# Kernel optimization log

Measured on AMD Instinct MI355X. Metric: run time of the kernel, lower is better.

## Reference

```python
import jax, jax.numpy as jnp
import numpy as np

BOUND = 5.0      # zuko MonotonicRQSTransform default bound
SLOPE = 1e-4     # minimum derivative slope
BINS = 5
HIDDEN = [128, 128, 128, 128]
N = 524288


def setup_inputs() -> dict:
    key = jax.random.key(0)
    ks = jax.random.split(key, 16)
    x = jax.random.normal(ks[0], (N, 1), dtype=jnp.float32)   # context
    z = jax.random.normal(ks[1], (N, 1), dtype=jnp.float32)   # base-normal sample
    dims = [1] + HIDDEN + [3 * BINS - 1]  # conditioner MLP: 1 -> 128x4 -> 14
    inp = {"x": x, "z": z}
    for i, (din, dout) in enumerate(zip(dims[:-1], dims[1:])):
        inp[f"W{i}"] = jax.random.normal(ks[2 + 2 * i], (din, dout), jnp.float32) / np.sqrt(din).astype(np.float32)
        inp[f"b{i}"] = jax.random.normal(ks[3 + 2 * i], (dout,), jnp.float32) * 0.01
    return inp


def _mlp(c, Ws, bs):
    h = c
    for W, b in zip(Ws[:-1], bs[:-1]):
        h = jax.nn.relu(h @ W + b)
    return h @ Ws[-1] + bs[-1]


def _rqs_inverse(z, w_raw, h_raw, d_raw):
    """Inverse of the monotonic rational-quadratic spline (Durkan et al. 2019).
    z: [N]; w_raw,h_raw: [N,K]; d_raw: [N,K-1]. Identity outside [-B, B]."""
    widths = 2.0 * BOUND * jax.nn.softmax(w_raw, axis=-1)
    heights = 2.0 * BOUND * jax.nn.softmax(h_raw, axis=-1)
    xk = -BOUND + jnp.pad(jnp.cumsum(widths, -1), ((0, 0), (1, 0)))   # [N,K+1] x-knots
    yk = -BOUND + jnp.pad(jnp.cumsum(heights, -1), ((0, 0), (1, 0)))  # [N,K+1] y-knots
    dk = jnp.pad(SLOPE + jax.nn.softplus(d_raw), ((0, 0), (1, 1)), constant_values=1.0)  # [N,K+1]

    zc = jnp.clip(z, -BOUND, BOUND)
    # bin search over K=5 inner knots via comparison-sum
    k = jnp.clip(jnp.sum(zc[:, None] >= yk[:, 1:-1], axis=-1), 0, BINS - 1)  # [N]
    take = lambda a: jnp.take_along_axis(a, k[:, None], axis=-1)[:, 0]
    x0, x1 = take(xk[:, :-1]), take(xk[:, 1:])
    y0, y1 = take(yk[:, :-1]), take(yk[:, 1:])
    d0, d1 = take(dk[:, :-1]), take(dk[:, 1:])

    dx, dy = x1 - x0, y1 - y0
    s = dy / dx
    t = zc - y0
    m = d0 + d1 - 2.0 * s
    a = dy * (s - d0) + t * m
    b = dy * d0 - t * m
    c = -s * t
    disc = jnp.maximum(b * b - 4.0 * a * c, 0.0)
    xi = 2.0 * c / (-b - jnp.sqrt(disc))  # stable quadratic root in [0,1]
    x_in = x0 + xi * dx
    return jnp.where(jnp.abs(z) >= BOUND, z, x_in)


def reference(x, z, W0, b0, W1, b1, W2, b2, W3, b3, W4, b4):
    # NICE with features=1: masks [T],[F],[T] -> transforms 0 & 2 are identity;
    # only transform 1 is active, conditioned on the context alone.
    Ws = [W0, W1, W2, W3, W4]
    bs = [b0, b1, b2, b3, b4]
    phi = _mlp(x, Ws, bs)  # [N, 3*BINS-1]
    w_raw = phi[:, :BINS]
    h_raw = phi[:, BINS:2 * BINS]
    d_raw = phi[:, 2 * BINS:]
    y = _rqs_inverse(z[:, 0], w_raw, h_raw, d_raw)  # sample = T^{-1}(z)
    return y[:, None]
```

## Files before the change

### kernel.cpp

```cpp
#include <hip/hip_runtime.h>

typedef _Float16 half8 __attribute__((ext_vector_type(8)));
typedef _Float16 half2v __attribute__((ext_vector_type(2)));
typedef __fp16   fp16x2 __attribute__((ext_vector_type(2)));
typedef float    f32x4 __attribute__((ext_vector_type(4)));


__global__ __launch_bounds__(256) void prep_kernel(
    const float* __restrict__ W1, const float* __restrict__ W2,
    const float* __restrict__ W3, const float* __restrict__ W4,
    const float* __restrict__ W0, const float* __restrict__ b0,
    _Float16* __restrict__ out)
{
    int t = blockIdx.x * blockDim.x + threadIdx.x;
    if (t >= 6912) return;
    int lane = t & 63;
    int frag = t >> 6;
    int col  = lane & 15;
    int kq   = (lane >> 4) << 2;

    if (frag < 96) {
        int l = frag >> 5, f = frag & 31;
        const float* W = (l == 0) ? W1 : (l == 1) ? W2 : W3;
        int mt = f >> 2, ks = f & 3;
        _Float16* dst = out + l * 16384 + f * 512 + lane * 8;
        int m = mt * 16 + col;
        int kbase = ks * 32 + kq;
#pragma unroll
        for (int j = 0; j < 8; ++j) {
            int k = kbase + 16 * (j >> 2) + (j & 3);
            dst[j] = (_Float16)W[k * 128 + m];
        }
    } else if (frag < 100) {
        int ks = frag - 96;
        _Float16* dst = out + 49152 + ks * 512 + lane * 8;
        int m = col;
        int kbase = ks * 32 + kq;
#pragma unroll
        for (int j = 0; j < 8; ++j) {
            int k = kbase + 16 * (j >> 2) + (j & 3);
            float v = (m < 14) ? W4[k * 14 + m] : 0.0f;
            dst[j] = (_Float16)v;
        }
    } else {
        int mt = frag - 100;
        _Float16* dst = out + 53248 + mt * 512 + lane * 8;
        int m = mt * 16 + col;
#pragma unroll
        for (int j = 0; j < 8; ++j) {
            int k = 16 * (j >> 2) + kq + (j & 3);
            float v = (k == 0) ? W0[m] : (k == 1) ? b0[m] : 0.0f;
            dst[j] = (_Float16)v;
        }
    }
}

static __device__ __forceinline__ half2v relu_cvt2(float a, float b) {
    fp16x2 h = __builtin_amdgcn_cvt_pkrtz(a, b);
    fp16x2 zz = {(__fp16)0.0f, (__fp16)0.0f};
    h = __builtin_elementwise_max(h, zz);
    return __builtin_bit_cast(half2v, h);
}

static __device__ __forceinline__ void hidden_layer(
    const half8 (&bin)[4][4], half8 (&bout)[4][4],
    const float* __restrict__ bias, const _Float16* __restrict__ Al,
    int lane, int quad)
{
#pragma unroll
    for (int mtp = 0; mtp < 4; ++mtp) {
        f32x4 acc[4][2];
        half8 a[2][4];
#pragma unroll
        for (int h = 0; h < 2; ++h) {
            int mt = 2 * mtp + h;
            f32x4 bv = *(const f32x4*)(bias + mt * 16 + quad * 4);
#pragma unroll
            for (int g = 0; g < 4; ++g) acc[g][h] = bv;
#pragma unroll
            for (int ks = 0; ks < 4; ++ks)
                a[h][ks] = *(const half8*)(Al + (mt * 4 + ks) * 512 + lane * 8);
        }
        __builtin_amdgcn_s_setprio(1);
#pragma unroll
        for (int h = 0; h < 2; ++h)
#pragma unroll
            for (int ks = 0; ks < 4; ++ks)
#pragma unroll
                for (int g = 0; g < 4; ++g)
                    acc[g][h] = __builtin_amdgcn_mfma_f32_16x16x32_f16(a[h][ks], bin[g][ks], acc[g][h], 0, 0, 0);
        __builtin_amdgcn_s_setprio(0);
#pragma unroll
        for (int g = 0; g < 4; ++g) {
            half2v p0 = relu_cvt2(acc[g][0][0], acc[g][0][1]);
            half2v p1 = relu_cvt2(acc[g][0][2], acc[g][0][3]);
            half2v p2 = relu_cvt2(acc[g][1][0], acc[g][1][1]);
            half2v p3 = relu_cvt2(acc[g][1][2], acc[g][1][3]);
            bout[g][mtp][0] = p0[0]; bout[g][mtp][1] = p0[1];
            bout[g][mtp][2] = p1[0]; bout[g][mtp][3] = p1[1];
            bout[g][mtp][4] = p2[0]; bout[g][mtp][5] = p2[1];
            bout[g][mtp][6] = p3[0]; bout[g][mtp][7] = p3[1];
        }
    }
}

__global__ __launch_bounds__(256, 2) void nflow_kernel(
    const float* __restrict__ x, const float* __restrict__ z,
    const float* __restrict__ b1, const float* __restrict__ b2,
    const float* __restrict__ b3, const float* __restrict__ b4v,
    const _Float16* __restrict__ Af, float* __restrict__ y, int N)
{
    __shared__ float phis[256][20];

    const int tid  = threadIdx.x;
    const int lane = tid & 63;
    const int wid  = tid >> 6;
    const int col  = lane & 15;
    const int quad = lane >> 4;
    const int sbase = blockIdx.x * 256 + wid * 64;

    half8 bufA[4][4], bufB[4][4];

    {
        half8 bx[4];
#pragma unroll
        for (int g = 0; g < 4; ++g) {
            int s = sbase + g * 16 + col;
            float xv = (s < N) ? x[s] : 0.0f;
            half8 t = {};
            if (quad == 0) { t[0] = (_Float16)xv; t[1] = (_Float16)1.0f; }
            bx[g] = t;
        }
#pragma unroll
        for (int mtp = 0; mtp < 4; ++mtp) {
            f32x4 acc[4][2];
            half8 a[2];
#pragma unroll
            for (int h = 0; h < 2; ++h)
                a[h] = *(const half8*)(Af + 53248 + (2 * mtp + h) * 512 + lane * 8);
            __builtin_amdgcn_s_setprio(1);
#pragma unroll
            for (int h = 0; h < 2; ++h)
#pragma unroll
                for (int g = 0; g < 4; ++g)
                    acc[g][h] = __builtin_amdgcn_mfma_f32_16x16x32_f16(a[h], bx[g], (f32x4){0.f,0.f,0.f,0.f}, 0, 0, 0);
            __builtin_amdgcn_s_setprio(0);
#pragma unroll
            for (int g = 0; g < 4; ++g) {
                half2v p0 = relu_cvt2(acc[g][0][0], acc[g][0][1]);
                half2v p1 = relu_cvt2(acc[g][0][2], acc[g][0][3]);
                half2v p2 = relu_cvt2(acc[g][1][0], acc[g][1][1]);
                half2v p3 = relu_cvt2(acc[g][1][2], acc[g][1][3]);
                bufA[g][mtp][0] = p0[0]; bufA[g][mtp][1] = p0[1];
                bufA[g][mtp][2] = p1[0]; bufA[g][mtp][3] = p1[1];
                bufA[g][mtp][4] = p2[0]; bufA[g][mtp][5] = p2[1];
                bufA[g][mtp][6] = p3[0]; bufA[g][mtp][7] = p3[1];
            }
        }
    }

    hidden_layer(bufA, bufB, b1, Af,         lane, quad);
    hidden_layer(bufB, bufA, b2, Af + 16384, lane, quad);
    hidden_layer(bufA, bufB, b3, Af + 32768, lane, quad);

    {
        f32x4 acc4[4];
        f32x4 binit;
#pragma unroll
        for (int r = 0; r < 4; ++r) {
            int comp = quad * 4 + r;
            binit[r] = (comp < 14) ? b4v[comp] : 0.0f;
        }
#pragma unroll
        for (int g = 0; g < 4; ++g) acc4[g] = binit;
        __builtin_amdgcn_s_setprio(1);
#pragma unroll
        for (int ks = 0; ks < 4; ++ks) {
            half8 a = *(const half8*)(Af + 49152 + ks * 512 + lane * 8);
#pragma unroll
            for (int g = 0; g < 4; ++g)
                acc4[g] = __builtin_amdgcn_mfma_f32_16x16x32_f16(a, bufB[g][ks], acc4[g], 0, 0, 0);
        }
        __builtin_amdgcn_s_setprio(0);
#pragma unroll
        for (int g = 0; g < 4; ++g)
            *(f32x4*)&phis[wid * 64 + g * 16 + col][quad * 4] = acc4[g];
    }

    __syncthreads();

    {
        int gs = blockIdx.x * 256 + tid;
        if (gs < N) {
            float ph[16];
            *(f32x4*)&ph[0]  = *(const f32x4*)&phis[tid][0];
            *(f32x4*)&ph[4]  = *(const f32x4*)&phis[tid][4];
            *(f32x4*)&ph[8]  = *(const f32x4*)&phis[tid][8];
            *(f32x4*)&ph[12] = *(const f32x4*)&phis[tid][12];

            float mw = ph[0], mh = ph[5];
#pragma unroll
            for (int i = 1; i < 5; ++i) { mw = fmaxf(mw, ph[i]); mh = fmaxf(mh, ph[5 + i]); }
            float ew[5], eh[5];
            float sw = 0.f, sh = 0.f;
#pragma unroll
            for (int i = 0; i < 5; ++i) {
                ew[i] = __expf(ph[i] - mw);      sw += ew[i];
                eh[i] = __expf(ph[5 + i] - mh);  sh += eh[i];
            }
            float iw = 10.0f / sw, ih = 10.0f / sh;
            float xk[6], yk[6], dk[6];
            xk[0] = -5.0f; yk[0] = -5.0f;
#pragma unroll
            for (int i = 0; i < 5; ++i) {
                xk[i + 1] = xk[i] + ew[i] * iw;
                yk[i + 1] = yk[i] + eh[i] * ih;
            }
            dk[0] = 1.0f; dk[5] = 1.0f;
#pragma unroll
            for (int i = 0; i < 4; ++i) {
                float v = ph[10 + i];
                dk[i + 1] = 0.0001f + fmaxf(v, 0.0f) + __logf(1.0f + __expf(-fabsf(v)));
            }
            float zv = z[gs];
            float zc = fminf(fmaxf(zv, -5.0f), 5.0f);
            int k = 0;
#pragma unroll
            for (int i = 1; i <= 4; ++i) k += (zc >= yk[i]) ? 1 : 0;
            float x0 = xk[0], x1 = xk[1], y0 = yk[0], y1 = yk[1], d0 = dk[0], d1 = dk[1];
#pragma unroll
            for (int i = 1; i < 5; ++i)
                if (k == i) { x0 = xk[i]; x1 = xk[i + 1]; y0 = yk[i]; y1 = yk[i + 1]; d0 = dk[i]; d1 = dk[i + 1]; }
            float dx = x1 - x0, dy = y1 - y0;
            float s  = dy / dx;
            float tt = zc - y0;
            float mm = d0 + d1 - 2.0f * s;
            float aa = dy * (s - d0) + tt * mm;
            float bb2 = dy * d0 - tt * mm;
            float cc = -s * tt;
            float disc = fmaxf(bb2 * bb2 - 4.0f * aa * cc, 0.0f);
            float xi   = (2.0f * cc) / (-bb2 - sqrtf(disc));
            float xin  = x0 + xi * dx;
            y[gs] = (fabsf(zv) >= 5.0f) ? zv : xin;
        }
    }
}

extern "C" void kernel_launch(void* const* d_in, const int* in_sizes, int n_in,
                              void* d_out, int out_size, void* d_ws, size_t ws_size,
                              hipStream_t stream) {
    const float* x  = (const float*)d_in[0];
    const float* z  = (const float*)d_in[1];
    const float* W0 = (const float*)d_in[2];
    const float* b0 = (const float*)d_in[3];
    const float* W1 = (const float*)d_in[4];
    const float* b1 = (const float*)d_in[5];
    const float* W2 = (const float*)d_in[6];
    const float* b2 = (const float*)d_in[7];
    const float* W3 = (const float*)d_in[8];
    const float* b3 = (const float*)d_in[9];
    const float* W4 = (const float*)d_in[10];
    const float* b4 = (const float*)d_in[11];
    float* y = (float*)d_out;
    int N = in_sizes[0];

    _Float16* wsH = (_Float16*)d_ws;
    prep_kernel<<<27, 256, 0, stream>>>(W1, W2, W3, W4, W0, b0, wsH);
    int nblk = (N + 255) / 256;
    nflow_kernel<<<nblk, 256, 0, stream>>>(x, z, b1, b2, b3, b4, wsH, y, N);
}
```

Baseline: 124.8 us.

## Stage MLP weights in LDS and run persistent 512-thread blocks

Each block now copies the whole packed fp16 weight buffer, about 110 KB, into shared memory once. It launches a fixed grid of 256 blocks of 512 threads, and each block loops over 4 chunks of 512 samples, reading MFMA A-fragments from LDS instead of global memory. The first-layer weight offset is compacted to fit the LDS array, and the s_setprio hints are removed. This aims to cut repeated global/L1 traffic for the weights, but it limits the CU to one large block with barriers each iteration, and the hard-coded grid only covers N up to 524288.

```diff
diff --git a/kernel.cpp b/kernel.cpp
--- a/kernel.cpp
+++ b/kernel.cpp
@@ -44,7 +44,7 @@
         }
     } else {
         int mt = frag - 100;
-        _Float16* dst = out + 53248 + mt * 512 + lane * 8;
+        _Float16* dst = out + 51200 + mt * 512 + lane * 8;
         int m = mt * 16 + col;
 #pragma unroll
         for (int j = 0; j < 8; ++j) {
@@ -64,7 +64,7 @@
 
 static __device__ __forceinline__ void hidden_layer(
     const half8 (&bin)[4][4], half8 (&bout)[4][4],
-    const float* __restrict__ bias, const _Float16* __restrict__ Al,
+    const float* __restrict__ bias, const _Float16* Al,
     int lane, int quad)
 {
 #pragma unroll
@@ -81,7 +81,6 @@
             for (int ks = 0; ks < 4; ++ks)
                 a[h][ks] = *(const half8*)(Al + (mt * 4 + ks) * 512 + lane * 8);
         }
-        __builtin_amdgcn_s_setprio(1);
 #pragma unroll
         for (int h = 0; h < 2; ++h)
 #pragma unroll
@@ -89,7 +88,6 @@
 #pragma unroll
                 for (int g = 0; g < 4; ++g)
                     acc[g][h] = __builtin_amdgcn_mfma_f32_16x16x32_f16(a[h][ks], bin[g][ks], acc[g][h], 0, 0, 0);
-        __builtin_amdgcn_s_setprio(0);
 #pragma unroll
         for (int g = 0; g < 4; ++g) {
             half2v p0 = relu_cvt2(acc[g][0][0], acc[g][0][1]);
@@ -104,93 +102,97 @@
     }
 }
 
-__global__ __launch_bounds__(256, 2) void nflow_kernel(
+__global__ __launch_bounds__(512, 2) void nflow_kernel(
     const float* __restrict__ x, const float* __restrict__ z,
     const float* __restrict__ b1, const float* __restrict__ b2,
     const float* __restrict__ b3, const float* __restrict__ b4v,
     const _Float16* __restrict__ Af, float* __restrict__ y, int N)
 {
-    __shared__ float phis[256][20];
+    __shared__ _Float16 wlds[55296];
+    __shared__ float phis[512][16];
 
     const int tid  = threadIdx.x;
     const int lane = tid & 63;
     const int wid  = tid >> 6;
     const int col  = lane & 15;
     const int quad = lane >> 4;
-    const int sbase = blockIdx.x * 256 + wid * 64;
-
-    half8 bufA[4][4], bufB[4][4];
-
-    {
-        half8 bx[4];
-#pragma unroll
-        for (int g = 0; g < 4; ++g) {
-            int s = sbase + g * 16 + col;
-            float xv = (s < N) ? x[s] : 0.0f;
-            half8 t = {};
-            if (quad == 0) { t[0] = (_Float16)xv; t[1] = (_Float16)1.0f; }
-            bx[g] = t;
-        }
-#pragma unroll
-        for (int mtp = 0; mtp < 4; ++mtp) {
-            f32x4 acc[4][2];
-            half8 a[2];
-#pragma unroll
-            for (int h = 0; h < 2; ++h)
-                a[h] = *(const half8*)(Af + 53248 + (2 * mtp + h) * 512 + lane * 8);
-            __builtin_amdgcn_s_setprio(1);
-#pragma unroll
-            for (int h = 0; h < 2; ++h)
+    const int base0 = blockIdx.x * 2048;
+
+    for (int c = tid; c < 6912; c += 512)
+        *(half8*)&wlds[c * 8] = *(const half8*)(Af + c * 8);
+    __syncthreads();
+
+    for (int it = 0; it < 4; ++it) {
+        const int sbase = base0 + it * 512 + wid * 64;
+        const int gs    = base0 + it * 512 + tid;
+        float zv = (gs < N) ? z[gs] : 0.0f;
+
+        half8 bufA[4][4], bufB[4][4];
+
+        {
+            half8 bx[4];
+#pragma unroll
+            for (int g = 0; g < 4; ++g) {
+                int s = sbase + g * 16 + col;
+                float xv = (s < N) ? x[s] : 0.0f;
+                half8 t = {};
+                if (quad == 0) { t[0] = (_Float16)xv; t[1] = (_Float16)1.0f; }
+                bx[g] = t;
+            }
+#pragma unroll
+            for (int mtp = 0; mtp < 4; ++mtp) {
+                f32x4 acc[4][2];
+                half8 a[2];
+#pragma unroll
+                for (int h = 0; h < 2; ++h)
+                    a[h] = *(const half8*)(&wlds[51200 + (2 * mtp + h) * 512 + lane * 8]);
+#pragma unroll
+                for (int h = 0; h < 2; ++h)
+#pragma unroll
+                    for (int g = 0; g < 4; ++g)
+                        acc[g][h] = __builtin_amdgcn_mfma_f32_16x16x32_f16(a[h], bx[g], (f32x4){0.f,0.f,0.f,0.f}, 0, 0, 0);
+#pragma unroll
+                for (int g = 0; g < 4; ++g) {
+                    half2v p0 = relu_cvt2(acc[g][0][0], acc[g][0][1]);
+                    half2v p1 = relu_cvt2(acc[g][0][2], acc[g][0][3]);
+                    half2v p2 = relu_cvt2(acc[g][1][0], acc[g][1][1]);
+                    half2v p3 = relu_cvt2(acc[g][1][2], acc[g][1][3]);
+                    bufA[g][mtp][0] = p0[0]; bufA[g][mtp][1] = p0[1];
+                    bufA[g][mtp][2] = p1[0]; bufA[g][mtp][3] = p1[1];
+                    bufA[g][mtp][4] = p2[0]; bufA[g][mtp][5] = p2[1];
+                    bufA[g][mtp][6] = p3[0]; bufA[g][mtp][7] = p3[1];
+                }
+            }
+        }
+
+        hidden_layer(bufA, bufB, b1, &wlds[0],     lane, quad);
+        hidden_layer(bufB, bufA, b2, &wlds[16384], lane, quad);
+        hidden_layer(bufA, bufB, b3, &wlds[32768], lane, quad);
+
+        {
+            f32x4 acc4[4];
+            f32x4 binit;
+#pragma unroll
+            for (int r = 0; r < 4; ++r) {
+                int comp = quad * 4 + r;
+                binit[r] = (comp < 14) ? b4v[comp] : 0.0f;
+            }
+#pragma unroll
+            for (int g = 0; g < 4; ++g) acc4[g] = binit;
+#pragma unroll
+            for (int ks = 0; ks < 4; ++ks) {
+                half8 a = *(const half8*)(&wlds[49152 + ks * 512 + lane * 8]);
 #pragma unroll
                 for (int g = 0; g < 4; ++g)
-                    acc[g][h] = __builtin_amdgcn_mfma_f32_16x16x32_f16(a[h], bx[g], (f32x4){0.f,0.f,0.f,0.f}, 0, 0, 0);
-            __builtin_amdgcn_s_setprio(0);
-#pragma unroll
-            for (int g = 0; g < 4; ++g) {
-                half2v p0 = relu_cvt2(acc[g][0][0], acc[g][0][1]);
-                half2v p1 = relu_cvt2(acc[g][0][2], acc[g][0][3]);
-                half2v p2 = relu_cvt2(acc[g][1][0], acc[g][1][1]);
-                half2v p3 = relu_cvt2(acc[g][1][2], acc[g][1][3]);
-                bufA[g][mtp][0] = p0[0]; bufA[g][mtp][1] = p0[1];
-                bufA[g][mtp][2] = p1[0]; bufA[g][mtp][3] = p1[1];
-                bufA[g][mtp][4] = p2[0]; bufA[g][mtp][5] = p2[1];
-                bufA[g][mtp][6] = p3[0]; bufA[g][mtp][7] = p3[1];
-            }
-        }
-    }
-
-    hidden_layer(bufA, bufB, b1, Af,         lane, quad);
-    hidden_layer(bufB, bufA, b2, Af + 16384, lane, quad);
-    hidden_layer(bufA, bufB, b3, Af + 32768, lane, quad);
-
-    {
-        f32x4 acc4[4];
-        f32x4 binit;
-#pragma unroll
-        for (int r = 0; r < 4; ++r) {
-            int comp = quad * 4 + r;
-            binit[r] = (comp < 14) ? b4v[comp] : 0.0f;
-        }
-#pragma unroll
-        for (int g = 0; g < 4; ++g) acc4[g] = binit;
-        __builtin_amdgcn_s_setprio(1);
-#pragma unroll
-        for (int ks = 0; ks < 4; ++ks) {
-            half8 a = *(const half8*)(Af + 49152 + ks * 512 + lane * 8);
+                    acc4[g] = __builtin_amdgcn_mfma_f32_16x16x32_f16(a, bufB[g][ks], acc4[g], 0, 0, 0);
+            }
 #pragma unroll
             for (int g = 0; g < 4; ++g)
-                acc4[g] = __builtin_amdgcn_mfma_f32_16x16x32_f16(a, bufB[g][ks], acc4[g], 0, 0, 0);
-        }
-        __builtin_amdgcn_s_setprio(0);
-#pragma unroll
-        for (int g = 0; g < 4; ++g)
-            *(f32x4*)&phis[wid * 64 + g * 16 + col][quad * 4] = acc4[g];
-    }
-
-    __syncthreads();
-
-    {
-        int gs = blockIdx.x * 256 + tid;
+                *(f32x4*)&phis[wid * 64 + g * 16 + col][quad * 4] = acc4[g];
+        }
+
+        __syncthreads();
+
         if (gs < N) {
             float ph[16];
             *(f32x4*)&ph[0]  = *(const f32x4*)&phis[tid][0];
@@ -222,7 +224,6 @@
                 float v = ph[10 + i];
                 dk[i + 1] = 0.0001f + fmaxf(v, 0.0f) + __logf(1.0f + __expf(-fabsf(v)));
             }
-            float zv = z[gs];
             float zc = fminf(fmaxf(zv, -5.0f), 5.0f);
             int k = 0;
 #pragma unroll
@@ -243,6 +244,8 @@
             float xin  = x0 + xi * dx;
             y[gs] = (fabsf(zv) >= 5.0f) ? zv : xin;
         }
+
+        __syncthreads();
     }
 }
 
@@ -266,6 +269,5 @@
 
     _Float16* wsH = (_Float16*)d_ws;
     prep_kernel<<<27, 256, 0, stream>>>(W1, W2, W3, W4, W0, b0, wsH);
-    int nblk = (N + 255) / 256;
-    nflow_kernel<<<nblk, 256, 0, stream>>>(x, z, b1, b2, b3, b4, wsH, y, N);
-}
+    nflow_kernel<<<256, 512, 0, stream>>>(x, z, b1, b2, b3, b4, wsH, y, N);
+}
```

Result: slower. 144.3 us (+15.7%).

## Software-pipeline weight fragment loads across MFMA stages with double-buffered registers

Applied to the files above, without the earlier changes.

Restructures the hidden-layer loop into explicit per-stage load and MFMA steps, using two register stages so the next stage's weight fragments and bias are fetched while the current stage's MFMAs run, including across layer boundaries. The bias is now passed as the first MFMA's accumulator input, the z load and the first-layer and last-layer weights are hoisted early, and the packed layer-0 weights move to a compacted offset. The s_setprio hints are dropped. Extra live register stages raise VGPR pressure, which at launch bounds of 256x2 could cause spills or reduce occupancy.

```diff
diff --git a/kernel.cpp b/kernel.cpp
--- a/kernel.cpp
+++ b/kernel.cpp
@@ -44,7 +44,7 @@
         }
     } else {
         int mt = frag - 100;
-        _Float16* dst = out + 53248 + mt * 512 + lane * 8;
+        _Float16* dst = out + 51200 + mt * 512 + lane * 8;
         int m = mt * 16 + col;
 #pragma unroll
         for (int j = 0; j < 8; ++j) {
@@ -62,46 +62,50 @@
     return __builtin_bit_cast(half2v, h);
 }
 
-static __device__ __forceinline__ void hidden_layer(
-    const half8 (&bin)[4][4], half8 (&bout)[4][4],
-    const float* __restrict__ bias, const _Float16* __restrict__ Al,
+struct Stage {
+    half8 a[2][4];
+    f32x4 bv[2];
+};
+
+template<int MTP>
+static __device__ __forceinline__ void load_stage(
+    Stage& s, const _Float16* __restrict__ Al, const float* __restrict__ bias,
     int lane, int quad)
 {
 #pragma unroll
-    for (int mtp = 0; mtp < 4; ++mtp) {
-        f32x4 acc[4][2];
-        half8 a[2][4];
-#pragma unroll
-        for (int h = 0; h < 2; ++h) {
-            int mt = 2 * mtp + h;
-            f32x4 bv = *(const f32x4*)(bias + mt * 16 + quad * 4);
-#pragma unroll
-            for (int g = 0; g < 4; ++g) acc[g][h] = bv;
-#pragma unroll
-            for (int ks = 0; ks < 4; ++ks)
-                a[h][ks] = *(const half8*)(Al + (mt * 4 + ks) * 512 + lane * 8);
-        }
-        __builtin_amdgcn_s_setprio(1);
-#pragma unroll
-        for (int h = 0; h < 2; ++h)
-#pragma unroll
-            for (int ks = 0; ks < 4; ++ks)
-#pragma unroll
-                for (int g = 0; g < 4; ++g)
-                    acc[g][h] = __builtin_amdgcn_mfma_f32_16x16x32_f16(a[h][ks], bin[g][ks], acc[g][h], 0, 0, 0);
-        __builtin_amdgcn_s_setprio(0);
-#pragma unroll
-        for (int g = 0; g < 4; ++g) {
-            half2v p0 = relu_cvt2(acc[g][0][0], acc[g][0][1]);
-            half2v p1 = relu_cvt2(acc[g][0][2], acc[g][0][3]);
-            half2v p2 = relu_cvt2(acc[g][1][0], acc[g][1][1]);
-            half2v p3 = relu_cvt2(acc[g][1][2], acc[g][1][3]);
-            bout[g][mtp][0] = p0[0]; bout[g][mtp][1] = p0[1];
-            bout[g][mtp][2] = p1[0]; bout[g][mtp][3] = p1[1];
-            bout[g][mtp][4] = p2[0]; bout[g][mtp][5] = p2[1];
-            bout[g][mtp][6] = p3[0]; bout[g][mtp][7] = p3[1];
-        }
-    }
+    for (int hh = 0; hh < 2; ++hh) {
+#pragma unroll
+        for (int ks = 0; ks < 4; ++ks)
+            s.a[hh][ks] = *(const half8*)(Al + ((2 * MTP + hh) * 4 + ks) * 512 + lane * 8);
+        s.bv[hh] = *(const f32x4*)(bias + (2 * MTP + hh) * 16 + quad * 4);
+    }
+}
+
+template<int MTP>
+static __device__ __forceinline__ void mfma_stage(
+    const half8 (&bin)[4][4], half8 (&bout)[4][4], const Stage& s)
+{
+    f32x4 acc[4][2];
+#pragma unroll
+    for (int hh = 0; hh < 2; ++hh)
+#pragma unroll
+        for (int g = 0; g < 4; ++g)
+            acc[g][hh] = __builtin_amdgcn_mfma_f32_16x16x32_f16(s.a[hh][0], bin[g][0], s.bv[hh], 0, 0, 0);
+#pragma unroll
+    for (int ks = 1; ks < 4; ++ks)
+#pragma unroll
+        for (int hh = 0; hh < 2; ++hh)
+#pragma unroll
+            for (int g = 0; g < 4; ++g)
+                acc[g][hh] = __builtin_amdgcn_mfma_f32_16x16x32_f16(s.a[hh][ks], bin[g][ks], acc[g][hh], 0, 0, 0);
+#pragma unroll
+    for (int g = 0; g < 4; ++g)
+#pragma unroll
+        for (int p = 0; p < 4; ++p) {
+            half2v hv = relu_cvt2(acc[g][p >> 1][2 * (p & 1)], acc[g][p >> 1][2 * (p & 1) + 1]);
+            bout[g][MTP][2 * p]     = hv[0];
+            bout[g][MTP][2 * p + 1] = hv[1];
+        }
 }
 
 __global__ __launch_bounds__(256, 2) void nflow_kernel(
@@ -118,70 +122,99 @@
     const int col  = lane & 15;
     const int quad = lane >> 4;
     const int sbase = blockIdx.x * 256 + wid * 64;
-
-    half8 bufA[4][4], bufB[4][4];
-
-    {
-        half8 bx[4];
-#pragma unroll
-        for (int g = 0; g < 4; ++g) {
-            int s = sbase + g * 16 + col;
-            float xv = (s < N) ? x[s] : 0.0f;
-            half8 t = {};
-            if (quad == 0) { t[0] = (_Float16)xv; t[1] = (_Float16)1.0f; }
-            bx[g] = t;
-        }
-#pragma unroll
-        for (int mtp = 0; mtp < 4; ++mtp) {
-            f32x4 acc[4][2];
-            half8 a[2];
-#pragma unroll
-            for (int h = 0; h < 2; ++h)
-                a[h] = *(const half8*)(Af + 53248 + (2 * mtp + h) * 512 + lane * 8);
-            __builtin_amdgcn_s_setprio(1);
-#pragma unroll
-            for (int h = 0; h < 2; ++h)
-#pragma unroll
-                for (int g = 0; g < 4; ++g)
-                    acc[g][h] = __builtin_amdgcn_mfma_f32_16x16x32_f16(a[h], bx[g], (f32x4){0.f,0.f,0.f,0.f}, 0, 0, 0);
-            __builtin_amdgcn_s_setprio(0);
-#pragma unroll
-            for (int g = 0; g < 4; ++g) {
-                half2v p0 = relu_cvt2(acc[g][0][0], acc[g][0][1]);
-                half2v p1 = relu_cvt2(acc[g][0][2], acc[g][0][3]);
-                half2v p2 = relu_cvt2(acc[g][1][0], acc[g][1][1]);
-                half2v p3 = relu_cvt2(acc[g][1][2], acc[g][1][3]);
-                bufA[g][mtp][0] = p0[0]; bufA[g][mtp][1] = p0[1];
-                bufA[g][mtp][2] = p1[0]; bufA[g][mtp][3] = p1[1];
-                bufA[g][mtp][4] = p2[0]; bufA[g][mtp][5] = p2[1];
-                bufA[g][mtp][6] = p3[0]; bufA[g][mtp][7] = p3[1];
+    const int gs    = blockIdx.x * 256 + tid;
+
+    float zv = (gs < N) ? z[gs] : 0.0f;
+
+    const _Float16* A1 = Af;
+    const _Float16* A2 = Af + 16384;
+    const _Float16* A3 = Af + 32768;
+
+    half8 aL0[8];
+#pragma unroll
+    for (int mt = 0; mt < 8; ++mt)
+        aL0[mt] = *(const half8*)(Af + 51200 + mt * 512 + lane * 8);
+
+    half8 bx[4];
+#pragma unroll
+    for (int g = 0; g < 4; ++g) {
+        int s = sbase + g * 16 + col;
+        float xv = (s < N) ? x[s] : 0.0f;
+        half8 t = {};
+        if (quad == 0) { t[0] = (_Float16)xv; t[1] = (_Float16)1.0f; }
+        bx[g] = t;
+    }
+
+    Stage sA, sB;
+    load_stage<0>(sA, A1, b1, lane, quad);
+
+    half8 binA[4][4], binB[4][4];
+
+    const f32x4 zero4 = {0.f, 0.f, 0.f, 0.f};
+#pragma unroll
+    for (int mtp = 0; mtp < 4; ++mtp) {
+        f32x4 acc[4][2];
+#pragma unroll
+        for (int hh = 0; hh < 2; ++hh)
+#pragma unroll
+            for (int g = 0; g < 4; ++g)
+                acc[g][hh] = __builtin_amdgcn_mfma_f32_16x16x32_f16(aL0[2 * mtp + hh], bx[g], zero4, 0, 0, 0);
+#pragma unroll
+        for (int g = 0; g < 4; ++g)
+#pragma unroll
+            for (int p = 0; p < 4; ++p) {
+                half2v hv = relu_cvt2(acc[g][p >> 1][2 * (p & 1)], acc[g][p >> 1][2 * (p & 1) + 1]);
+                binA[g][mtp][2 * p]     = hv[0];
+                binA[g][mtp][2 * p + 1] = hv[1];
             }
-        }
-    }
-
-    hidden_layer(bufA, bufB, b1, Af,         lane, quad);
-    hidden_layer(bufB, bufA, b2, Af + 16384, lane, quad);
-    hidden_layer(bufA, bufB, b3, Af + 32768, lane, quad);
+    }
+
+    load_stage<1>(sB, A1, b1, lane, quad);
+    mfma_stage<0>(binA, binB, sA);
+    load_stage<2>(sA, A1, b1, lane, quad);
+    mfma_stage<1>(binA, binB, sB);
+    load_stage<3>(sB, A1, b1, lane, quad);
+    mfma_stage<2>(binA, binB, sA);
+    load_stage<0>(sA, A2, b2, lane, quad);
+    mfma_stage<3>(binA, binB, sB);
+
+    load_stage<1>(sB, A2, b2, lane, quad);
+    mfma_stage<0>(binB, binA, sA);
+    load_stage<2>(sA, A2, b2, lane, quad);
+    mfma_stage<1>(binB, binA, sB);
+    load_stage<3>(sB, A2, b2, lane, quad);
+    mfma_stage<2>(binB, binA, sA);
+    load_stage<0>(sA, A3, b3, lane, quad);
+    mfma_stage<3>(binB, binA, sB);
+
+    load_stage<1>(sB, A3, b3, lane, quad);
+    mfma_stage<0>(binA, binB, sA);
+    load_stage<2>(sA, A3, b3, lane, quad);
+    mfma_stage<1>(binA, binB, sB);
+    load_stage<3>(sB, A3, b3, lane, quad);
+    mfma_stage<2>(binA, binB, sA);
+    half8 a4[4];
+#pragma unroll
+    for (int ks = 0; ks < 4; ++ks)
+        a4[ks] = *(const half8*)(Af + 49152 + ks * 512 + lane * 8);
+    f32x4 b4init;
+#pragma unroll
+    for (int r = 0; r < 4; ++r) {
+        int comp = quad * 4 + r;
+        b4init[r] = (comp < 14) ? b4v[comp] : 0.0f;
+    }
+    mfma_stage<3>(binA, binB, sB);
 
     {
         f32x4 acc4[4];
-        f32x4 binit;
-#pragma unroll
-        for (int r = 0; r < 4; ++r) {
-            int comp = quad * 4 + r;
-            binit[r] = (comp < 14) ? b4v[comp] : 0.0f;
-        }
-#pragma unroll
-        for (int g = 0; g < 4; ++g) acc4[g] = binit;
-        __builtin_amdgcn_s_setprio(1);
-#pragma unroll
-        for (int ks = 0; ks < 4; ++ks) {
-            half8 a = *(const half8*)(Af + 49152 + ks * 512 + lane * 8);
+#pragma unroll
+        for (int g = 0; g < 4; ++g)
+            acc4[g] = __builtin_amdgcn_mfma_f32_16x16x32_f16(a4[0], binB[g][0], b4init, 0, 0, 0);
+#pragma unroll
+        for (int ks = 1; ks < 4; ++ks)
 #pragma unroll
             for (int g = 0; g < 4; ++g)
-                acc4[g] = __builtin_amdgcn_mfma_f32_16x16x32_f16(a, bufB[g][ks], acc4[g], 0, 0, 0);
-        }
-        __builtin_amdgcn_s_setprio(0);
+                acc4[g] = __builtin_amdgcn_mfma_f32_16x16x32_f16(a4[ks], binB[g][ks], acc4[g], 0, 0, 0);
 #pragma unroll
         for (int g = 0; g < 4; ++g)
             *(f32x4*)&phis[wid * 64 + g * 16 + col][quad * 4] = acc4[g];
@@ -189,60 +222,56 @@
 
     __syncthreads();
 
-    {
-        int gs = blockIdx.x * 256 + tid;
-        if (gs < N) {
-            float ph[16];
-            *(f32x4*)&ph[0]  = *(const f32x4*)&phis[tid][0];
-            *(f32x4*)&ph[4]  = *(const f32x4*)&phis[tid][4];
-            *(f32x4*)&ph[8]  = *(const f32x4*)&phis[tid][8];
-            *(f32x4*)&ph[12] = *(const f32x4*)&phis[tid][12];
-
-            float mw = ph[0], mh = ph[5];
-#pragma unroll
-            for (int i = 1; i < 5; ++i) { mw = fmaxf(mw, ph[i]); mh = fmaxf(mh, ph[5 + i]); }
-            float ew[5], eh[5];
-            float sw = 0.f, sh = 0.f;
-#pragma unroll
-            for (int i = 0; i < 5; ++i) {
-                ew[i] = __expf(ph[i] - mw);      sw += ew[i];
-                eh[i] = __expf(ph[5 + i] - mh);  sh += eh[i];
-            }
-            float iw = 10.0f / sw, ih = 10.0f / sh;
-            float xk[6], yk[6], dk[6];
-            xk[0] = -5.0f; yk[0] = -5.0f;
-#pragma unroll
-            for (int i = 0; i < 5; ++i) {
-                xk[i + 1] = xk[i] + ew[i] * iw;
-                yk[i + 1] = yk[i] + eh[i] * ih;
-            }
-            dk[0] = 1.0f; dk[5] = 1.0f;
-#pragma unroll
-            for (int i = 0; i < 4; ++i) {
-                float v = ph[10 + i];
-                dk[i + 1] = 0.0001f + fmaxf(v, 0.0f) + __logf(1.0f + __expf(-fabsf(v)));
-            }
-            float zv = z[gs];
-            float zc = fminf(fmaxf(zv, -5.0f), 5.0f);
-            int k = 0;
-#pragma unroll
-            for (int i = 1; i <= 4; ++i) k += (zc >= yk[i]) ? 1 : 0;
-            float x0 = xk[0], x1 = xk[1], y0 = yk[0], y1 = yk[1], d0 = dk[0], d1 = dk[1];
-#pragma unroll
-            for (int i = 1; i < 5; ++i)
-                if (k == i) { x0 = xk[i]; x1 = xk[i + 1]; y0 = yk[i]; y1 = yk[i + 1]; d0 = dk[i]; d1 = dk[i + 1]; }
-            float dx = x1 - x0, dy = y1 - y0;
-            float s  = dy / dx;
-            float tt = zc - y0;
-            float mm = d0 + d1 - 2.0f * s;
-            float aa = dy * (s - d0) + tt * mm;
-            float bb2 = dy * d0 - tt * mm;
-            float cc = -s * tt;
-            float disc = fmaxf(bb2 * bb2 - 4.0f * aa * cc, 0.0f);
-            float xi   = (2.0f * cc) / (-bb2 - sqrtf(disc));
-            float xin  = x0 + xi * dx;
-            y[gs] = (fabsf(zv) >= 5.0f) ? zv : xin;
-        }
+    if (gs < N) {
+        float ph[16];
+        *(f32x4*)&ph[0]  = *(const f32x4*)&phis[tid][0];
+        *(f32x4*)&ph[4]  = *(const f32x4*)&phis[tid][4];
+        *(f32x4*)&ph[8]  = *(const f32x4*)&phis[tid][8];
+        *(f32x4*)&ph[12] = *(const f32x4*)&phis[tid][12];
+
+        float mw = ph[0], mh = ph[5];
+#pragma unroll
+        for (int i = 1; i < 5; ++i) { mw = fmaxf(mw, ph[i]); mh = fmaxf(mh, ph[5 + i]); }
+        float ew[5], eh[5];
+        float sw = 0.f, sh = 0.f;
+#pragma unroll
+        for (int i = 0; i < 5; ++i) {
+            ew[i] = __expf(ph[i] - mw);      sw += ew[i];
+            eh[i] = __expf(ph[5 + i] - mh);  sh += eh[i];
+        }
+        float iw = 10.0f / sw, ih = 10.0f / sh;
+        float xk[6], yk[6], dk[6];
+        xk[0] = -5.0f; yk[0] = -5.0f;
+#pragma unroll
+        for (int i = 0; i < 5; ++i) {
+            xk[i + 1] = xk[i] + ew[i] * iw;
+            yk[i + 1] = yk[i] + eh[i] * ih;
+        }
+        dk[0] = 1.0f; dk[5] = 1.0f;
+#pragma unroll
+        for (int i = 0; i < 4; ++i) {
+            float v = ph[10 + i];
+            dk[i + 1] = 0.0001f + fmaxf(v, 0.0f) + __logf(1.0f + __expf(-fabsf(v)));
+        }
+        float zc = fminf(fmaxf(zv, -5.0f), 5.0f);
+        int k = 0;
+#pragma unroll
+        for (int i = 1; i <= 4; ++i) k += (zc >= yk[i]) ? 1 : 0;
+        float x0 = xk[0], x1 = xk[1], y0 = yk[0], y1 = yk[1], d0 = dk[0], d1 = dk[1];
+#pragma unroll
+        for (int i = 1; i < 5; ++i)
+            if (k == i) { x0 = xk[i]; x1 = xk[i + 1]; y0 = yk[i]; y1 = yk[i + 1]; d0 = dk[i]; d1 = dk[i + 1]; }
+        float dx = x1 - x0, dy = y1 - y0;
+        float s  = dy / dx;
+        float tt = zc - y0;
+        float mm = d0 + d1 - 2.0f * s;
+        float aa = dy * (s - d0) + tt * mm;
+        float bb2 = dy * d0 - tt * mm;
+        float cc = -s * tt;
+        float disc = fmaxf(bb2 * bb2 - 4.0f * aa * cc, 0.0f);
+        float xi   = (2.0f * cc) / (-bb2 - sqrtf(disc));
+        float xin  = x0 + xi * dx;
+        y[gs] = (fabsf(zv) >= 5.0f) ? zv : xin;
     }
 }
 
```

Result: slower. 129.4 us (+3.7%).
